# Kernel tuning notes

Hardware: AMD Instinct MI355X
Metric: run time of the kernel (lower is better)

The kernel has to match this reference:

```python
import jax, jax.numpy as jnp
import numpy as np

N = 100000       # nodes
E = 1600000      # edges (avg degree 16)
D_IN = 128
D_HID = 32
D_OUT = 32
H = 4            # heads
NEG_SLOPE = 0.2  # GATConv default leaky_relu slope


def setup_inputs() -> dict:
    key = jax.random.key(0)
    ks = jax.random.split(key, 10)
    s = 0.1
    return {
        "edge": jax.random.randint(ks[0], (2, E), 0, N),
        "features": jax.random.normal(ks[1], (N, D_IN), jnp.float32),
        # layer 1 params: W [in, H*hid], attention vectors per head [H, hid]
        "W1": jax.random.normal(ks[2], (D_IN, H * D_HID), jnp.float32) * s,
        "a1_src": jax.random.normal(ks[3], (H, D_HID), jnp.float32) * s,
        "a1_dst": jax.random.normal(ks[4], (H, D_HID), jnp.float32) * s,
        "b1": jnp.zeros((H * D_HID,), jnp.float32),
        # layer 2 params
        "W2": jax.random.normal(ks[5], (H * D_HID, H * D_OUT), jnp.float32) * s,
        "a2_src": jax.random.normal(ks[6], (H, D_OUT), jnp.float32) * s,
        "a2_dst": jax.random.normal(ks[7], (H, D_OUT), jnp.float32) * s,
        "b2": jnp.zeros((H * D_OUT,), jnp.float32),
    }


def gat_conv(x, src, dst, W, a_src, a_dst, b, heads, d_out):
    """Multi-head GAT layer, concat heads. x: [N, d_in] -> [N, heads*d_out]."""
    n = x.shape[0]
    h = (x @ W).reshape(n, heads, d_out)                 # [N,H,D]
    e_src = jnp.einsum('nhd,hd->nh', h, a_src)           # [N,H]
    e_dst = jnp.einsum('nhd,hd->nh', h, a_dst)           # [N,H]
    e = jax.nn.leaky_relu(e_src[src] + e_dst[dst], NEG_SLOPE)  # [E,H]
    # softmax over incoming edges of each dst node (stable via segment max)
    m = jax.lax.stop_gradient(jax.ops.segment_max(e, dst, num_segments=n))
    w = jnp.exp(e - m[dst])                              # [E,H]
    den = jax.ops.segment_sum(w, dst, num_segments=n)    # [N,H]
    alpha = w / den[dst]                                 # [E,H]
    out = jax.ops.segment_sum(alpha[:, :, None] * h[src], dst, num_segments=n)
    return out.reshape(n, heads * d_out) + b


def reference(edge, features, W1, a1_src, a1_dst, b1, W2, a2_src, a2_dst, b2):
    src, dst = edge[0], edge[1]
    h = jax.nn.relu(gat_conv(features, src, dst, W1, a1_src, a1_dst, b1, H, D_HID))
    h = gat_conv(h, src, dst, W2, a2_src, a2_dst, b2, H, D_OUT)
    return jax.nn.log_softmax(h, axis=1)
```

## Files before the change

kernel.cpp:

```cpp
#include <hip/hip_runtime.h>
#include <hip/hip_bf16.h>
#include <math.h>

#define N_NODES 100000
#define N_EDGES 1600000
#define NHEADS 4
#define NEG_SLOPE 0.2f
#define NB 1563
#define KSUB 8
#define SUBCAP 224
#define BCAPT (KSUB * SUBCAP)
#define CPAD 32

typedef __attribute__((ext_vector_type(8))) short short8;
typedef __attribute__((ext_vector_type(4))) float f32x4;
typedef __attribute__((ext_vector_type(2))) float f32x2;

__device__ __forceinline__ unsigned short f2bf(float f) {
    unsigned int u = __float_as_uint(f);
    u += 0x7fffu + ((u >> 16) & 1u);
    return (unsigned short)(u >> 16);
}
__device__ __forceinline__ float bf_lo(unsigned int u) {
    return __uint_as_float(u << 16);
}
__device__ __forceinline__ float bf_hi(unsigned int u) {
    return __uint_as_float(u & 0xffff0000u);
}
__device__ __forceinline__ f32x2 bfpair(unsigned int u) {
    f32x2 r;
    r.x = __uint_as_float(u << 16);
    r.y = __uint_as_float(u & 0xffff0000u);
    return r;
}
__device__ __forceinline__ short8 pack8(float4 f0, float4 f1) {
    short8 v;
    v[0] = (short)f2bf(f0.x); v[1] = (short)f2bf(f0.y);
    v[2] = (short)f2bf(f0.z); v[3] = (short)f2bf(f0.w);
    v[4] = (short)f2bf(f1.x); v[5] = (short)f2bf(f1.y);
    v[6] = (short)f2bf(f1.z); v[7] = (short)f2bf(f1.w);
    return v;
}

__global__ void pack_w_kernel(const float* __restrict__ W,
                              const float* __restrict__ a_src,
                              const float* __restrict__ a_dst,
                              unsigned short* __restrict__ Wp) {
    int idx = blockIdx.x * 256 + threadIdx.x;
    if (idx >= 18432) return;
    int j    = idx & 7;
    int lane = (idx >> 3) & 63;
    int kc   = (idx >> 9) & 3;
    int ct   = idx >> 11;
    int k = kc * 32 + ((lane >> 4) & 3) * 8 + j;
    int n = lane & 15;
    float v = 0.f;
    if (ct < 8) {
        v = W[k * 128 + ct * 16 + n];
    } else if (n < 8) {
        int hd = n & 3;
        const float* av = (n < 4 ? a_src : a_dst) + hd * 32;
        const float* wr = W + k * 128 + hd * 32;
#pragma unroll
        for (int t = 0; t < 32; ++t) v = fmaf(wr[t], av[t], v);
    }
    Wp[idx] = f2bf(v);
}

template <bool XF32>
__global__ __launch_bounds__(256) void gemm_mfma_kernel(
        const void* __restrict__ xv,
        const unsigned short* __restrict__ Wp,
        unsigned short* __restrict__ h, float* __restrict__ esd, int n_rows) {
    __shared__ unsigned short Wl[18432];

    const int t = threadIdx.x;
    {
        const uint4* s4 = (const uint4*)Wp;
        uint4* d4 = (uint4*)Wl;
#pragma unroll
        for (int p = 0; p < 9; ++p) d4[p * 256 + t] = s4[p * 256 + t];
    }
    __syncthreads();

    const int lane = t & 63, wave = t >> 6;
    const int l15 = lane & 15, quad = lane >> 4;
    const int rbase = blockIdx.x * 128 + wave * 32;

    short8 a[2][4];
#pragma unroll
    for (int rt = 0; rt < 2; ++rt) {
        int r = rbase + rt * 16 + l15;
        r = r < n_rows ? r : n_rows - 1;
        if (XF32) {
            const float* xr = (const float*)xv + (size_t)r * 128 + quad * 8;
#pragma unroll
            for (int kc = 0; kc < 4; ++kc) {
                float4 f0 = *(const float4*)(xr + kc * 32);
                float4 f1 = *(const float4*)(xr + kc * 32 + 4);
                a[rt][kc] = pack8(f0, f1);
            }
        } else {
            const unsigned short* xr =
                (const unsigned short*)xv + (size_t)r * 128 + quad * 8;
#pragma unroll
            for (int kc = 0; kc < 4; ++kc)
                a[rt][kc] = *(const short8*)(xr + kc * 32);
        }
    }

    f32x4 acc[2][9];
#pragma unroll
    for (int rt = 0; rt < 2; ++rt)
#pragma unroll
        for (int ct = 0; ct < 9; ++ct)
            acc[rt][ct] = (f32x4){0.f, 0.f, 0.f, 0.f};

#pragma unroll
    for (int ct = 0; ct < 9; ++ct) {
#pragma unroll
        for (int kc = 0; kc < 4; ++kc) {
            short8 b = *(const short8*)&Wl[((ct * 4 + kc) * 64 + lane) * 8];
            acc[0][ct] = __builtin_amdgcn_mfma_f32_16x16x32_bf16(
                a[0][kc], b, acc[0][ct], 0, 0, 0);
            acc[1][ct] = __builtin_amdgcn_mfma_f32_16x16x32_bf16(
                a[1][kc], b, acc[1][ct], 0, 0, 0);
        }
    }

#pragma unroll
    for (int rt = 0; rt < 2; ++rt) {
#pragma unroll
        for (int i = 0; i < 4; ++i) {
            int r = rbase + rt * 16 + quad * 4 + i;
            if (r < n_rows) {
                unsigned short* hp = h + (size_t)r * 128 + l15;
#pragma unroll
                for (int ct = 0; ct < 8; ++ct)
                    hp[ct * 16] = f2bf(acc[rt][ct][i]);
                if (l15 < 8) esd[r * 8 + l15] = acc[rt][8][i];
            }
        }
    }
}

__global__ void zero_ints_kernel(int* __restrict__ p, int n) {
    int i = blockIdx.x * 256 + threadIdx.x;
    if (i < n) p[i] = 0;
}

__global__ void bucket_fill_kernel(const int* __restrict__ src,
                                   const int* __restrict__ dst,
                                   int* __restrict__ bcnt,
                                   unsigned int* __restrict__ slab) {
    int e = blockIdx.x * 256 + threadIdx.x;
    if (e >= N_EDGES) return;
    int d = dst[e];
    int b = d >> 6;
    int sub = blockIdx.x & (KSUB - 1);
    int c = b * KSUB + sub;
    int pos = atomicAdd(&bcnt[c * CPAD], 1);
    slab[(size_t)b * BCAPT + sub * SUBCAP + pos] =
        (unsigned int)src[e] | ((unsigned int)(d & 63) << 17);
}

__global__ __launch_bounds__(256) void bucket_hist_kernel(
        const int* __restrict__ bcnt, const unsigned int* __restrict__ slab,
        int* __restrict__ deg) {
    __shared__ int hist[64];
    const int b = blockIdx.x;
    if (threadIdx.x < 64) hist[threadIdx.x] = 0;
    __syncthreads();
    const int lane = threadIdx.x & 63, wave = threadIdx.x >> 6;
    const unsigned int* sp = slab + (size_t)b * BCAPT;
#pragma unroll
    for (int s = wave; s < KSUB; s += 4) {
        const int m = bcnt[(b * KSUB + s) * CPAD];
        for (int i = lane; i < m; i += 64)
            atomicAdd(&hist[sp[s * SUBCAP + i] >> 17], 1);
    }
    __syncthreads();
    if (threadIdx.x < 64) {
        int node = b * 64 + threadIdx.x;
        if (node < N_NODES) deg[node] = hist[threadIdx.x];
    }
}

__global__ __launch_bounds__(256) void scan1_kernel(const int* __restrict__ deg,
                                                    int* __restrict__ rowptr,
                                                    int* __restrict__ partials) {
    __shared__ int wsum[4];
    int i = blockIdx.x * 256 + threadIdx.x;
    int lane = threadIdx.x & 63, wave = threadIdx.x >> 6;
    int orig = (i < N_NODES) ? deg[i] : 0;
    int v = orig;
#pragma unroll
    for (int off = 1; off < 64; off <<= 1) {
        int t = __shfl_up(v, off);
        if (lane >= off) v += t;
    }
    if (lane == 63) wsum[wave] = v;
    __syncthreads();
    int woff = 0;
#pragma unroll
    for (int w = 0; w < 4; ++w) if (w < wave) woff += wsum[w];
    if (i < N_NODES) rowptr[i] = v - orig + woff;
    if (threadIdx.x == 0)
        partials[blockIdx.x] = wsum[0] + wsum[1] + wsum[2] + wsum[3];
}

__global__ __launch_bounds__(512) void scan2_kernel(int* __restrict__ partials,
                                                    int nb) {
    __shared__ int wsum[8];
    int i = threadIdx.x;
    int lane = i & 63, wave = i >> 6;
    int orig = (i < nb) ? partials[i] : 0;
    int v = orig;
#pragma unroll
    for (int off = 1; off < 64; off <<= 1) {
        int t = __shfl_up(v, off);
        if (lane >= off) v += t;
    }
    if (lane == 63) wsum[wave] = v;
    __syncthreads();
    int woff = 0;
#pragma unroll
    for (int w = 0; w < 8; ++w) if (w < wave) woff += wsum[w];
    if (i < nb) partials[i] = v - orig + woff;
}

__global__ void scan3_kernel(int* __restrict__ rowptr,
                             const int* __restrict__ partials) {
    int i = blockIdx.x * 256 + threadIdx.x;
    if (i < N_NODES) rowptr[i] += partials[blockIdx.x];
}

__global__ __launch_bounds__(256) void bucket_scatter_kernel(
        const int* __restrict__ bcnt, const unsigned int* __restrict__ slab,
        const int* __restrict__ rowptr, int* __restrict__ csr_src) {
    __shared__ int rp[64];
    __shared__ int cnt[64];
    const int b = blockIdx.x;
    if (threadIdx.x < 64) {
        int node = b * 64 + threadIdx.x;
        rp[threadIdx.x] = node < N_NODES ? rowptr[node] : 0;
        cnt[threadIdx.x] = 0;
    }
    __syncthreads();
    const int lane = threadIdx.x & 63, wave = threadIdx.x >> 6;
    const unsigned int* sp = slab + (size_t)b * BCAPT;
#pragma unroll
    for (int s = wave; s < KSUB; s += 4) {
        const int m = bcnt[(b * KSUB + s) * CPAD];
        for (int i = lane; i < m; i += 64) {
            unsigned int rec = sp[s * SUBCAP + i];
            int local = rec >> 17;
            int pos = rp[local] + atomicAdd(&cnt[local], 1);
            csr_src[pos] = (int)(rec & 0x1FFFFu);
        }
    }
}

template <bool LOGSOFTMAX>
__global__ __launch_bounds__(256) void aggregate_kernel(
        const int* __restrict__ csr_src, const int* __restrict__ rowptr,
        const int* __restrict__ deg, const float* __restrict__ esd,
        const unsigned short* __restrict__ hb, const float* __restrict__ b,
        void* __restrict__ out) {
    const int lane = threadIdx.x & 63;
    const int wave = threadIdx.x >> 6;
    const int n = blockIdx.x * 4 + wave;
    if (n >= N_NODES) return;
    const int eo = lane >> 4;
    const int cl = lane & 15;
    const int c0 = cl * 8;
    const int hd = cl >> 2;
    const float edn = esd[n * 8 + 4 + hd];
    const int base = rowptr[n];
    const int dg = deg[n];

    f32x2 acc2[4];
#pragma unroll
    for (int j = 0; j < 4; ++j) acc2[j] = (f32x2){0.f, 0.f};
    float wsum = 0.f;

    if (dg > 0) {
        const int myidx = csr_src[base + (lane < dg ? lane : dg - 1)];
        const int nit = (dg + 3) >> 2;
        const unsigned hbo = (unsigned)c0 * 2u;
        const unsigned edo = (unsigned)hd * 4u;
        const char* hbp = (const char*)hb;
        const char* esp = (const char*)esd;

        auto getS = [&](int j) -> int {
            int o = 4 * j + eo;
            if (4 * j < 64) return __shfl(myidx, o);
            int oc = o < dg ? o : dg - 1;
            return csr_src[base + oc];
        };
        auto loadP = [&](int s) -> uint4 {
            return *(const uint4*)(hbp + (((unsigned)s << 8) + hbo));
        };
        auto loadE = [&](int s, int j) -> float {
            float e = *(const float*)(esp + (((unsigned)s << 5) + edo));
            return (4 * j + eo < dg) ? e : -1e30f;
        };

        int s0 = getS(0);
        uint4 p0 = loadP(s0);
        float e0 = loadE(s0, 0);
        uint4 p1 = p0; float e1 = e0;
        if (nit > 1) {
            int s1 = getS(1);
            p1 = loadP(s1);
            e1 = loadE(s1, 1);
        }
#pragma unroll 2
        for (int j = 0; j < nit; ++j) {
            uint4 p2 = p1; float e2 = e1;
            if (j + 2 < nit) {
                int s2 = getS(j + 2);
                p2 = loadP(s2);
                e2 = loadE(s2, j + 2);
            }
            float sc = e0 + edn;
            sc = sc > 0.f ? sc : NEG_SLOPE * sc;
            float w = __expf(sc);
            f32x2 wv = {w, w};
            acc2[0] = __builtin_elementwise_fma(wv, bfpair(p0.x), acc2[0]);
            acc2[1] = __builtin_elementwise_fma(wv, bfpair(p0.y), acc2[1]);
            acc2[2] = __builtin_elementwise_fma(wv, bfpair(p0.z), acc2[2]);
            acc2[3] = __builtin_elementwise_fma(wv, bfpair(p0.w), acc2[3]);
            wsum += w;
            p0 = p1; e0 = e1; p1 = p2; e1 = e2;
        }
    }

    float acc[8];
#pragma unroll
    for (int j = 0; j < 4; ++j) {
        acc[2 * j]     = acc2[j].x;
        acc[2 * j + 1] = acc2[j].y;
    }

#pragma unroll
    for (int j = 0; j < 8; ++j) {
        acc[j] += __shfl_xor(acc[j], 16);
        acc[j] += __shfl_xor(acc[j], 32);
    }
    wsum += __shfl_xor(wsum, 16);
    wsum += __shfl_xor(wsum, 32);

    float inv = wsum > 0.f ? 1.f / wsum : 0.f;
    float bl[8];
    *(float4*)&bl[0] = *(const float4*)(b + c0);
    *(float4*)&bl[4] = *(const float4*)(b + c0 + 4);
    float v[8];
#pragma unroll
    for (int j = 0; j < 8; ++j) v[j] = acc[j] * inv + bl[j];

    if (!LOGSOFTMAX) {
        if (lane < 16) {
            unsigned int pk[4];
#pragma unroll
            for (int j = 0; j < 4; ++j) {
                float r0 = v[2 * j]     > 0.f ? v[2 * j]     : 0.f;
                float r1 = v[2 * j + 1] > 0.f ? v[2 * j + 1] : 0.f;
                pk[j] = (unsigned int)f2bf(r0) | ((unsigned int)f2bf(r1) << 16);
            }
            *(uint4*)((unsigned short*)out + (size_t)n * 128 + c0) =
                make_uint4(pk[0], pk[1], pk[2], pk[3]);
        }
    } else {
        float m = v[0];
#pragma unroll
        for (int j = 1; j < 8; ++j) m = fmaxf(m, v[j]);
#pragma unroll
        for (int s = 1; s < 16; s <<= 1) m = fmaxf(m, __shfl_xor(m, s));
        float se = 0.f;
#pragma unroll
        for (int j = 0; j < 8; ++j) se += __expf(v[j] - m);
#pragma unroll
        for (int s = 1; s < 16; s <<= 1) se += __shfl_xor(se, s);
        float ls = m + logf(se);
        if (lane < 16) {
            float* o = (float*)out + (size_t)n * 128 + c0;
            *(float4*)o = make_float4(v[0] - ls, v[1] - ls, v[2] - ls, v[3] - ls);
            *(float4*)(o + 4) = make_float4(v[4] - ls, v[5] - ls, v[6] - ls, v[7] - ls);
        }
    }
}

extern "C" void kernel_launch(void* const* d_in, const int* in_sizes, int n_in,
                              void* d_out, int out_size, void* d_ws, size_t ws_size,
                              hipStream_t stream) {
    const int*   edge = (const int*)d_in[0];
    const int*   src  = edge;
    const int*   dst  = edge + N_EDGES;
    const float* feat = (const float*)d_in[1];
    const float* W1   = (const float*)d_in[2];
    const float* a1s  = (const float*)d_in[3];
    const float* a1d  = (const float*)d_in[4];
    const float* b1   = (const float*)d_in[5];
    const float* W2   = (const float*)d_in[6];
    const float* a2s  = (const float*)d_in[7];
    const float* a2d  = (const float*)d_in[8];
    const float* b2   = (const float*)d_in[9];
    float* out = (float*)d_out;

    unsigned short* hb  = (unsigned short*)d_ws;
    unsigned short* x1b = hb + (size_t)N_NODES * 128;
    unsigned short* Wp1 = x1b + (size_t)N_NODES * 128;
    unsigned short* Wp2 = Wp1 + 18432;
    float* esd = (float*)(Wp2 + 18432);
    int* deg      = (int*)(esd + (size_t)N_NODES * 8);
    int* rowptr   = deg + N_NODES;
    int* partials = rowptr + N_NODES;
    int* bcnt     = partials + 512;
    unsigned int* slab = (unsigned int*)(bcnt + NB * KSUB * CPAD);
    int* csr_src  = (int*)(slab + (size_t)NB * BCAPT);

    const int node_blk  = (N_NODES + 255) / 256;
    const int edge_blk  = (N_EDGES + 255) / 256;
    const int gemm_blk  = (N_NODES + 127) / 128;
    const int agg_blk   = (N_NODES + 3) / 4;
    const int nctr      = NB * KSUB * CPAD;

    zero_ints_kernel<<<(nctr + 255) / 256, 256, 0, stream>>>(bcnt, nctr);
    bucket_fill_kernel<<<edge_blk, 256, 0, stream>>>(src, dst, bcnt, slab);
    bucket_hist_kernel<<<NB, 256, 0, stream>>>(bcnt, slab, deg);
    scan1_kernel<<<node_blk, 256, 0, stream>>>(deg, rowptr, partials);
    scan2_kernel<<<1, 512, 0, stream>>>(partials, node_blk);
    scan3_kernel<<<node_blk, 256, 0, stream>>>(rowptr, partials);
    bucket_scatter_kernel<<<NB, 256, 0, stream>>>(bcnt, slab, rowptr, csr_src);

    pack_w_kernel<<<72, 256, 0, stream>>>(W1, a1s, a1d, Wp1);
    pack_w_kernel<<<72, 256, 0, stream>>>(W2, a2s, a2d, Wp2);

    gemm_mfma_kernel<true><<<gemm_blk, 256, 0, stream>>>(feat, Wp1, hb, esd, N_NODES);
    aggregate_kernel<false><<<agg_blk, 256, 0, stream>>>(
        csr_src, rowptr, deg, esd, hb, b1, x1b);

    gemm_mfma_kernel<false><<<gemm_blk, 256, 0, stream>>>(x1b, Wp2, hb, esd, N_NODES);
    aggregate_kernel<true><<<agg_blk, 256, 0, stream>>>(
        csr_src, rowptr, deg, esd, hb, b2, out);
}
```

Before: 394.9 us.

## Fuse CSR build: bucket-level scan plus combined histogram/scatter kernel

Replaces the five-kernel CSR construction (histogram, three-stage node scan, scatter) with a single-block scan over per-bucket totals followed by one kernel. That kernel builds each bucket's local histogram, scans it to produce rowptr, and scatters sources into CSR order. The degree array is dropped; aggregation derives degree from rowptr[n+1]-rowptr[n]. Edge index loads in the fill kernel become nontemporal. This cuts kernel launches and a second pass over the slab, at the cost of a serial single-block scan over about 1563 buckets.

```diff
diff --git a/kernel.cpp b/kernel.cpp
--- a/kernel.cpp
+++ b/kernel.cpp
@@ -20,12 +20,6 @@
     unsigned int u = __float_as_uint(f);
     u += 0x7fffu + ((u >> 16) & 1u);
     return (unsigned short)(u >> 16);
-}
-__device__ __forceinline__ float bf_lo(unsigned int u) {
-    return __uint_as_float(u << 16);
-}
-__device__ __forceinline__ float bf_hi(unsigned int u) {
-    return __uint_as_float(u & 0xffff0000u);
 }
 __device__ __forceinline__ f32x2 bfpair(unsigned int u) {
     f32x2 r;
@@ -155,23 +149,64 @@
                                    unsigned int* __restrict__ slab) {
     int e = blockIdx.x * 256 + threadIdx.x;
     if (e >= N_EDGES) return;
-    int d = dst[e];
+    int d = __builtin_nontemporal_load(dst + e);
+    int s = __builtin_nontemporal_load(src + e);
     int b = d >> 6;
     int sub = blockIdx.x & (KSUB - 1);
     int c = b * KSUB + sub;
     int pos = atomicAdd(&bcnt[c * CPAD], 1);
     slab[(size_t)b * BCAPT + sub * SUBCAP + pos] =
-        (unsigned int)src[e] | ((unsigned int)(d & 63) << 17);
-}
-
-__global__ __launch_bounds__(256) void bucket_hist_kernel(
+        (unsigned int)s | ((unsigned int)(d & 63) << 17);
+}
+
+__global__ __launch_bounds__(1024) void bucket_scan_kernel(
+        const int* __restrict__ bcnt, int* __restrict__ bbase,
+        int* __restrict__ rowptr) {
+    __shared__ int ws[16];
+    const int t = threadIdx.x;
+    const int lane = t & 63, wave = t >> 6;
+    if (t == 0) rowptr[N_NODES] = N_EDGES;
+    int carry = 0;
+#pragma unroll
+    for (int pass = 0; pass < 2; ++pass) {
+        int b = pass * 1024 + t;
+        int tot = 0;
+        if (b < NB) {
+#pragma unroll
+            for (int s = 0; s < KSUB; ++s) tot += bcnt[(b * KSUB + s) * CPAD];
+        }
+        int v = tot;
+#pragma unroll
+        for (int off = 1; off < 64; off <<= 1) {
+            int u = __shfl_up(v, off);
+            if (lane >= off) v += u;
+        }
+        if (lane == 63) ws[wave] = v;
+        __syncthreads();
+        int woff = 0, btot = 0;
+#pragma unroll
+        for (int w = 0; w < 16; ++w) {
+            if (w < wave) woff += ws[w];
+            btot += ws[w];
+        }
+        if (b < NB) bbase[b] = carry + woff + v - tot;
+        carry += btot;
+        __syncthreads();
+    }
+}
+
+__global__ __launch_bounds__(256) void bucket_build_kernel(
         const int* __restrict__ bcnt, const unsigned int* __restrict__ slab,
-        int* __restrict__ deg) {
+        const int* __restrict__ bbase, int* __restrict__ rowptr,
+        int* __restrict__ csr_src) {
     __shared__ int hist[64];
+    __shared__ int rp[64];
+    __shared__ int cnt[64];
     const int b = blockIdx.x;
-    if (threadIdx.x < 64) hist[threadIdx.x] = 0;
+    const int t = threadIdx.x;
+    if (t < 64) { hist[t] = 0; cnt[t] = 0; }
     __syncthreads();
-    const int lane = threadIdx.x & 63, wave = threadIdx.x >> 6;
+    const int lane = t & 63, wave = t >> 6;
     const unsigned int* sp = slab + (size_t)b * BCAPT;
 #pragma unroll
     for (int s = wave; s < KSUB; s += 4) {
@@ -180,75 +215,20 @@
             atomicAdd(&hist[sp[s * SUBCAP + i] >> 17], 1);
     }
     __syncthreads();
-    if (threadIdx.x < 64) {
-        int node = b * 64 + threadIdx.x;
-        if (node < N_NODES) deg[node] = hist[threadIdx.x];
-    }
-}
-
-__global__ __launch_bounds__(256) void scan1_kernel(const int* __restrict__ deg,
-                                                    int* __restrict__ rowptr,
-                                                    int* __restrict__ partials) {
-    __shared__ int wsum[4];
-    int i = blockIdx.x * 256 + threadIdx.x;
-    int lane = threadIdx.x & 63, wave = threadIdx.x >> 6;
-    int orig = (i < N_NODES) ? deg[i] : 0;
-    int v = orig;
-#pragma unroll
-    for (int off = 1; off < 64; off <<= 1) {
-        int t = __shfl_up(v, off);
-        if (lane >= off) v += t;
-    }
-    if (lane == 63) wsum[wave] = v;
+    if (wave == 0) {
+        int h = hist[lane];
+        int v = h;
+#pragma unroll
+        for (int off = 1; off < 64; off <<= 1) {
+            int u = __shfl_up(v, off);
+            if (lane >= off) v += u;
+        }
+        int r = bbase[b] + v - h;
+        rp[lane] = r;
+        int node = b * 64 + lane;
+        if (node < N_NODES) rowptr[node] = r;
+    }
     __syncthreads();
-    int woff = 0;
-#pragma unroll
-    for (int w = 0; w < 4; ++w) if (w < wave) woff += wsum[w];
-    if (i < N_NODES) rowptr[i] = v - orig + woff;
-    if (threadIdx.x == 0)
-        partials[blockIdx.x] = wsum[0] + wsum[1] + wsum[2] + wsum[3];
-}
-
-__global__ __launch_bounds__(512) void scan2_kernel(int* __restrict__ partials,
-                                                    int nb) {
-    __shared__ int wsum[8];
-    int i = threadIdx.x;
-    int lane = i & 63, wave = i >> 6;
-    int orig = (i < nb) ? partials[i] : 0;
-    int v = orig;
-#pragma unroll
-    for (int off = 1; off < 64; off <<= 1) {
-        int t = __shfl_up(v, off);
-        if (lane >= off) v += t;
-    }
-    if (lane == 63) wsum[wave] = v;
-    __syncthreads();
-    int woff = 0;
-#pragma unroll
-    for (int w = 0; w < 8; ++w) if (w < wave) woff += wsum[w];
-    if (i < nb) partials[i] = v - orig + woff;
-}
-
-__global__ void scan3_kernel(int* __restrict__ rowptr,
-                             const int* __restrict__ partials) {
-    int i = blockIdx.x * 256 + threadIdx.x;
-    if (i < N_NODES) rowptr[i] += partials[blockIdx.x];
-}
-
-__global__ __launch_bounds__(256) void bucket_scatter_kernel(
-        const int* __restrict__ bcnt, const unsigned int* __restrict__ slab,
-        const int* __restrict__ rowptr, int* __restrict__ csr_src) {
-    __shared__ int rp[64];
-    __shared__ int cnt[64];
-    const int b = blockIdx.x;
-    if (threadIdx.x < 64) {
-        int node = b * 64 + threadIdx.x;
-        rp[threadIdx.x] = node < N_NODES ? rowptr[node] : 0;
-        cnt[threadIdx.x] = 0;
-    }
-    __syncthreads();
-    const int lane = threadIdx.x & 63, wave = threadIdx.x >> 6;
-    const unsigned int* sp = slab + (size_t)b * BCAPT;
 #pragma unroll
     for (int s = wave; s < KSUB; s += 4) {
         const int m = bcnt[(b * KSUB + s) * CPAD];
@@ -264,7 +244,7 @@
 template <bool LOGSOFTMAX>
 __global__ __launch_bounds__(256) void aggregate_kernel(
         const int* __restrict__ csr_src, const int* __restrict__ rowptr,
-        const int* __restrict__ deg, const float* __restrict__ esd,
+        const float* __restrict__ esd,
         const unsigned short* __restrict__ hb, const float* __restrict__ b,
         void* __restrict__ out) {
     const int lane = threadIdx.x & 63;
@@ -277,7 +257,7 @@
     const int hd = cl >> 2;
     const float edn = esd[n * 8 + 4 + hd];
     const int base = rowptr[n];
-    const int dg = deg[n];
+    const int dg = rowptr[n + 1] - base;
 
     f32x2 acc2[4];
 #pragma unroll
@@ -413,14 +393,12 @@
     unsigned short* Wp1 = x1b + (size_t)N_NODES * 128;
     unsigned short* Wp2 = Wp1 + 18432;
     float* esd = (float*)(Wp2 + 18432);
-    int* deg      = (int*)(esd + (size_t)N_NODES * 8);
-    int* rowptr   = deg + N_NODES;
-    int* partials = rowptr + N_NODES;
-    int* bcnt     = partials + 512;
+    int* rowptr   = (int*)(esd + (size_t)N_NODES * 8);
+    int* bbase    = rowptr + (N_NODES + 1);
+    int* bcnt     = bbase + NB;
     unsigned int* slab = (unsigned int*)(bcnt + NB * KSUB * CPAD);
     int* csr_src  = (int*)(slab + (size_t)NB * BCAPT);
 
-    const int node_blk  = (N_NODES + 255) / 256;
     const int edge_blk  = (N_EDGES + 255) / 256;
     const int gemm_blk  = (N_NODES + 127) / 128;
     const int agg_blk   = (N_NODES + 3) / 4;
@@ -428,20 +406,17 @@
 
     zero_ints_kernel<<<(nctr + 255) / 256, 256, 0, stream>>>(bcnt, nctr);
     bucket_fill_kernel<<<edge_blk, 256, 0, stream>>>(src, dst, bcnt, slab);
-    bucket_hist_kernel<<<NB, 256, 0, stream>>>(bcnt, slab, deg);
-    scan1_kernel<<<node_blk, 256, 0, stream>>>(deg, rowptr, partials);
-    scan2_kernel<<<1, 512, 0, stream>>>(partials, node_blk);
-    scan3_kernel<<<node_blk, 256, 0, stream>>>(rowptr, partials);
-    bucket_scatter_kernel<<<NB, 256, 0, stream>>>(bcnt, slab, rowptr, csr_src);
+    bucket_scan_kernel<<<1, 1024, 0, stream>>>(bcnt, bbase, rowptr);
+    bucket_build_kernel<<<NB, 256, 0, stream>>>(bcnt, slab, bbase, rowptr, csr_src);
 
     pack_w_kernel<<<72, 256, 0, stream>>>(W1, a1s, a1d, Wp1);
     pack_w_kernel<<<72, 256, 0, stream>>>(W2, a2s, a2d, Wp2);
 
     gemm_mfma_kernel<true><<<gemm_blk, 256, 0, stream>>>(feat, Wp1, hb, esd, N_NODES);
     aggregate_kernel<false><<<agg_blk, 256, 0, stream>>>(
-        csr_src, rowptr, deg, esd, hb, b1, x1b);
+        csr_src, rowptr, esd, hb, b1, x1b);
 
     gemm_mfma_kernel<false><<<gemm_blk, 256, 0, stream>>>(x1b, Wp2, hb, esd, N_NODES);
     aggregate_kernel<true><<<agg_blk, 256, 0, stream>>>(
-        csr_src, rowptr, deg, esd, hb, b2, out);
-}
+        csr_src, rowptr, esd, hb, b2, out);
+}
```

Result: no change. 399.9 us (+1.3%).
